# Optimization experiments

Hardware: AMD Instinct MI355X
Metric: run time of the kernel (lower is better)

The kernel has to match this reference:

```python
import jax, jax.numpy as jnp
import numpy as np

B, TQ, TV = 16, 2048, 2048
DEC, ENC = 1024, 512

def setup_inputs() -> dict:
    key = jax.random.key(0)
    k1, k2, k3 = jax.random.split(key, 3)
    query = jax.random.normal(k1, (B, TQ, DEC), dtype=jnp.float32)
    value = jax.random.normal(k2, (B, TV, ENC), dtype=jnp.float32)
    # Dense(decoder_dim): kernel [ENC, DEC] + bias [DEC]
    W = jax.random.normal(k3, (ENC, DEC), dtype=jnp.float32) * (1.0 / np.sqrt(ENC))
    b = jnp.zeros((DEC,), dtype=jnp.float32)
    return {"query": query, "value": value, "W": W, "b": b}

def reference(query, value, W, b):
    # w(value): [B, TV, DEC]
    keys = jnp.einsum('bve,ed->bvd', value, W) + b
    # scores: query @ keys^T -> [B, TQ, TV]
    scores = jnp.einsum('bqd,bvd->bqv', query, keys)
    alignment = jax.nn.softmax(scores, axis=-1)
    # context: alignment @ value -> [B, TQ, ENC]
    context = jnp.einsum('bqv,bve->bqe', alignment, value)
    context = jnp.concatenate([context, query], axis=-1)  # [B, TQ, ENC+DEC]
    alignment_t = jnp.transpose(alignment, (0, 2, 1))      # [B, TV, TQ]
    return (context, alignment_t)
```

## Files before the change

kernel.cpp:

```cpp
#include <hip/hip_runtime.h>
#include <cstdint>
#include <cstddef>

typedef unsigned short u16;
typedef __bf16 bf16x8 __attribute__((ext_vector_type(8)));
typedef unsigned short u16x8 __attribute__((ext_vector_type(8)));
typedef unsigned short u16x4 __attribute__((ext_vector_type(4)));
typedef float f32x4 __attribute__((ext_vector_type(4)));

#define NB   16
#define TQ   2048
#define TV   2048
#define DDEC 1024
#define DENC 512
#define CTXW (DENC + DDEC)
#define CTXW2 (2*CTXW)

static __device__ __forceinline__ u16 f2bf(float f) {
    unsigned u = __builtin_bit_cast(unsigned, f);
    return (u16)((u + 0x7fffu + ((u >> 16) & 1u)) >> 16);
}
static __device__ __forceinline__ float bf2f(u16 h) {
    return __builtin_bit_cast(float, ((unsigned)h) << 16);
}

static __device__ __forceinline__ void stage_tile(
    u16* __restrict__ lds_tile, const u16* __restrict__ gsrc,
    int ldb, int w, int lane)
{
    #pragma unroll
    for (int p = 0; p < 2; ++p) {
        const int ci  = p * 4 + w;
        const int row = ci * 16 + (lane >> 2);
        const int col = (lane & 3) * 8;
        const u16* g = gsrc + (size_t)row * ldb + col;
        u16* l = lds_tile + ci * 512;
        __builtin_amdgcn_global_load_lds(
            (const __attribute__((address_space(1))) void*)g,
            (__attribute__((address_space(3))) void*)l, 16, 0, 0);
    }
}

__global__ __launch_bounds__(256)
void lk_prep_split(const float* __restrict__ X, u16* __restrict__ Xh, u16* __restrict__ Xl)
{
    const size_t i = ((size_t)blockIdx.x * 256 + threadIdx.x) * 4;
    const float4 v = *(const float4*)(X + i);
    const u16 h0=f2bf(v.x), h1=f2bf(v.y), h2=f2bf(v.z), h3=f2bf(v.w);
    u16x4 hv = {h0,h1,h2,h3};
    u16x4 lv = {f2bf(v.x-bf2f(h0)), f2bf(v.y-bf2f(h1)),
                f2bf(v.z-bf2f(h2)), f2bf(v.w-bf2f(h3))};
    *(u16x4*)(Xh + i) = hv;
    *(u16x4*)(Xl + i) = lv;
}

__global__ __launch_bounds__(256)
void lk_prep_vt(const float* __restrict__ V, u16* __restrict__ Vt)
{
    __shared__ float ts[32][36];
    const int t = threadIdx.x;
    const int r = t >> 3, c = (t & 7) * 4;
    const int e0 = blockIdx.x * 32, v0 = blockIdx.y * 32;
    const float* Vb = V + (size_t)blockIdx.z * TV * DENC;
    const float4 v = *(const float4*)(Vb + (size_t)(v0 + r) * DENC + e0 + c);
    *(float4*)&ts[r][c] = v;
    __syncthreads();
    u16x4 tv = { f2bf(ts[c+0][r]), f2bf(ts[c+1][r]),
                 f2bf(ts[c+2][r]), f2bf(ts[c+3][r]) };
    *(u16x4*)(Vt + (size_t)blockIdx.z * DENC * TV + (size_t)(e0 + r) * TV + v0 + c) = tv;
}

__global__ __launch_bounds__(256)
void lk_gemm_qw(const u16* __restrict__ Ah_g, const u16* __restrict__ Al_g,
                const u16* __restrict__ Bh_g, const u16* __restrict__ Bl_g,
                u16* __restrict__ Chi, u16* __restrict__ Clo)
{
    __shared__ u16 lAh[128*32], lAl[128*32], lBh[128*32], lBl[128*32];
    const int m0 = blockIdx.x * 128, n0 = blockIdx.y * 128;
    const int t = threadIdx.x;
    const int w = t >> 6, lane = t & 63, l15 = lane & 15, quad = lane >> 4;

    const u16* Ab_h = Ah_g + (size_t)m0 * DDEC;
    const u16* Ab_l = Al_g + (size_t)m0 * DDEC;
    const u16* Bb_h = Bh_g + (size_t)n0 * DDEC;
    const u16* Bb_l = Bl_g + (size_t)n0 * DDEC;

    f32x4 acc[2][8];
    #pragma unroll
    for (int i = 0; i < 2; ++i)
        #pragma unroll
        for (int j = 0; j < 8; ++j) acc[i][j] = (f32x4){0.f,0.f,0.f,0.f};

    for (int k0 = 0; k0 < DDEC; k0 += 32) {
        stage_tile(lAh, Ab_h + k0, DDEC, w, lane);
        stage_tile(lAl, Ab_l + k0, DDEC, w, lane);
        stage_tile(lBh, Bb_h + k0, DDEC, w, lane);
        stage_tile(lBl, Bb_l + k0, DDEC, w, lane);
        __syncthreads();
        bf16x8 ah[2], al[2];
        #pragma unroll
        for (int tm = 0; tm < 2; ++tm) {
            const int row = w*32 + tm*16 + l15;
            ah[tm] = __builtin_bit_cast(bf16x8, *(const u16x8*)&lAh[row*32 + quad*8]);
            al[tm] = __builtin_bit_cast(bf16x8, *(const u16x8*)&lAl[row*32 + quad*8]);
        }
        #pragma unroll
        for (int tn = 0; tn < 8; ++tn) {
            const int col = tn*16 + l15;
            const bf16x8 bh = __builtin_bit_cast(bf16x8, *(const u16x8*)&lBh[col*32 + quad*8]);
            const bf16x8 bl = __builtin_bit_cast(bf16x8, *(const u16x8*)&lBl[col*32 + quad*8]);
            #pragma unroll
            for (int tm = 0; tm < 2; ++tm) {
                acc[tm][tn] = __builtin_amdgcn_mfma_f32_16x16x32_bf16(ah[tm], bh, acc[tm][tn], 0,0,0);
                acc[tm][tn] = __builtin_amdgcn_mfma_f32_16x16x32_bf16(ah[tm], bl, acc[tm][tn], 0,0,0);
                acc[tm][tn] = __builtin_amdgcn_mfma_f32_16x16x32_bf16(al[tm], bh, acc[tm][tn], 0,0,0);
            }
        }
        __syncthreads();
    }
    #pragma unroll
    for (int tn = 0; tn < 8; ++tn) {
        const int col = n0 + tn*16 + l15;
        #pragma unroll
        for (int tm = 0; tm < 2; ++tm)
            #pragma unroll
            for (int r = 0; r < 4; ++r) {
                const int row = m0 + w*32 + tm*16 + quad*4 + r;
                const float c = acc[tm][tn][r];
                const u16 h = f2bf(c);
                Chi[(size_t)row*DENC + col] = h;
                Clo[(size_t)row*DENC + col] = f2bf(c - bf2f(h));
            }
    }
}

__global__ __launch_bounds__(256)
void lk_gemm_scores(const u16* __restrict__ Ah_g, const u16* __restrict__ Al_g,
                    const u16* __restrict__ Bh_g, const u16* __restrict__ Bl_g,
                    float* __restrict__ Sc, float2* __restrict__ sst)
{
    __shared__ u16 lAh[128*32], lAl[128*32], lBh[128*32], lBl[128*32];
    const int b = blockIdx.z;
    const int m0 = blockIdx.x * 128, n0 = blockIdx.y * 128;
    const int t = threadIdx.x;
    const int w = t >> 6, lane = t & 63, l15 = lane & 15, quad = lane >> 4;

    const u16* Ab_h = Ah_g + (size_t)b * TQ * DENC + (size_t)m0 * DENC;
    const u16* Ab_l = Al_g + (size_t)b * TQ * DENC + (size_t)m0 * DENC;
    const u16* Bb_h = Bh_g + (size_t)b * TV * DENC + (size_t)n0 * DENC;
    const u16* Bb_l = Bl_g + (size_t)b * TV * DENC + (size_t)n0 * DENC;

    f32x4 acc[2][8];
    #pragma unroll
    for (int i = 0; i < 2; ++i)
        #pragma unroll
        for (int j = 0; j < 8; ++j) acc[i][j] = (f32x4){0.f,0.f,0.f,0.f};

    for (int k0 = 0; k0 < DENC; k0 += 32) {
        stage_tile(lAh, Ab_h + k0, DENC, w, lane);
        stage_tile(lAl, Ab_l + k0, DENC, w, lane);
        stage_tile(lBh, Bb_h + k0, DENC, w, lane);
        stage_tile(lBl, Bb_l + k0, DENC, w, lane);
        __syncthreads();
        bf16x8 ah[2], al[2];
        #pragma unroll
        for (int tm = 0; tm < 2; ++tm) {
            const int row = w*32 + tm*16 + l15;
            ah[tm] = __builtin_bit_cast(bf16x8, *(const u16x8*)&lAh[row*32 + quad*8]);
            al[tm] = __builtin_bit_cast(bf16x8, *(const u16x8*)&lAl[row*32 + quad*8]);
        }
        #pragma unroll
        for (int tn = 0; tn < 8; ++tn) {
            const int col = tn*16 + l15;
            const bf16x8 bh = __builtin_bit_cast(bf16x8, *(const u16x8*)&lBh[col*32 + quad*8]);
            const bf16x8 bl = __builtin_bit_cast(bf16x8, *(const u16x8*)&lBl[col*32 + quad*8]);
            #pragma unroll
            for (int tm = 0; tm < 2; ++tm) {
                acc[tm][tn] = __builtin_amdgcn_mfma_f32_16x16x32_bf16(ah[tm], bh, acc[tm][tn], 0,0,0);
                acc[tm][tn] = __builtin_amdgcn_mfma_f32_16x16x32_bf16(ah[tm], bl, acc[tm][tn], 0,0,0);
                acc[tm][tn] = __builtin_amdgcn_mfma_f32_16x16x32_bf16(al[tm], bh, acc[tm][tn], 0,0,0);
            }
        }
        __syncthreads();
    }
    float* Sb = Sc + (size_t)b * TQ * TV;
    #pragma unroll
    for (int tm = 0; tm < 2; ++tm)
        #pragma unroll
        for (int tn = 0; tn < 8; ++tn) {
            const int col = n0 + tn*16 + l15;
            #pragma unroll
            for (int r = 0; r < 4; ++r) {
                const int row = m0 + w*32 + tm*16 + quad*4 + r;
                Sb[(size_t)row*TV + col] = acc[tm][tn][r];
            }
        }
    const int by = blockIdx.y;
    #pragma unroll
    for (int tm = 0; tm < 2; ++tm)
        #pragma unroll
        for (int r = 0; r < 4; ++r) {
            float m = acc[tm][0][r];
            #pragma unroll
            for (int tn = 1; tn < 8; ++tn) m = fmaxf(m, acc[tm][tn][r]);
            #pragma unroll
            for (int off = 1; off < 16; off <<= 1) m = fmaxf(m, __shfl_xor(m, off, 64));
            float s = 0.f;
            #pragma unroll
            for (int tn = 0; tn < 8; ++tn) s += __expf(acc[tm][tn][r] - m);
            #pragma unroll
            for (int off = 1; off < 16; off <<= 1) s += __shfl_xor(s, off, 64);
            if (l15 == 0) {
                const int row = m0 + w*32 + tm*16 + quad*4 + r;
                sst[((size_t)(b*16 + by))*TQ + row] = (float2){m, s};
            }
        }
}

__global__ __launch_bounds__(256)
void lk_combine(float2* __restrict__ sst)
{
    const int rg = blockIdx.x * 256 + threadIdx.x;
    const int b = rg >> 11, q = rg & (TQ - 1);
    float2* base = sst + (size_t)b * 16 * TQ;
    float2 v[16];
    float mx = -3.0e38f;
    #pragma unroll
    for (int y = 0; y < 16; ++y) {
        v[y] = base[(size_t)y * TQ + q];
        mx = fmaxf(mx, v[y].x);
    }
    float s = 0.f;
    #pragma unroll
    for (int y = 0; y < 16; ++y) s += v[y].y * __expf(v[y].x - mx);
    base[q] = (float2){mx, 1.0f / s};
}

__global__ __launch_bounds__(256)
void lk_norm_t(float* __restrict__ A, float* __restrict__ C,
               const float2* __restrict__ sstF)
{
    const int i = blockIdx.x, j = blockIdx.y;
    if (j < i) return;
    const int b = blockIdx.z;
    float* Ab = A + (size_t)b * TQ * TV;
    u16* Pb = (u16*)C + (size_t)b * TQ * CTXW2 + 2*DENC;
    const float2* st = sstF + (size_t)b * 16 * TQ;
    __shared__ float ta[32][36], tb[32][36];
    const int t = threadIdx.x;
    const int r = t >> 3, c = (t & 7) * 4;
    float* pij = Ab + (size_t)(i*32) * TV + j*32;
    float* pji = Ab + (size_t)(j*32) * TV + i*32;
    {
        const float2 s2 = st[i*32 + r];
        const float4 va = *(const float4*)(pij + (size_t)r * TV + c);
        float4 e = { __expf(va.x - s2.x) * s2.y, __expf(va.y - s2.x) * s2.y,
                     __expf(va.z - s2.x) * s2.y, __expf(va.w - s2.x) * s2.y };
        *(float4*)&ta[r][c] = e;
        u16x4 pv = {f2bf(e.x), f2bf(e.y), f2bf(e.z), f2bf(e.w)};
        *(u16x4*)(Pb + (size_t)(i*32 + r) * CTXW2 + j*32 + c) = pv;
    }
    if (i != j) {
        const float2 s2 = st[j*32 + r];
        const float4 vb = *(const float4*)(pji + (size_t)r * TV + c);
        float4 e = { __expf(vb.x - s2.x) * s2.y, __expf(vb.y - s2.x) * s2.y,
                     __expf(vb.z - s2.x) * s2.y, __expf(vb.w - s2.x) * s2.y };
        *(float4*)&tb[r][c] = e;
        u16x4 pv = {f2bf(e.x), f2bf(e.y), f2bf(e.z), f2bf(e.w)};
        *(u16x4*)(Pb + (size_t)(j*32 + r) * CTXW2 + i*32 + c) = pv;
    }
    __syncthreads();
    float4 oa = { ta[c+0][r], ta[c+1][r], ta[c+2][r], ta[c+3][r] };
    *(float4*)(pji + (size_t)r * TV + c) = oa;
    if (i != j) {
        float4 ob = { tb[c+0][r], tb[c+1][r], tb[c+2][r], tb[c+3][r] };
        *(float4*)(pij + (size_t)r * TV + c) = ob;
    }
}

__global__ __launch_bounds__(256)
void lk_gemm_ctx(const u16* __restrict__ Vt, float* C)
{
    __shared__ u16 lA[128*32], lB[128*32];
    const int b = blockIdx.z;
    const int m0 = blockIdx.x * 128, n0 = blockIdx.y * 128;
    const int t = threadIdx.x;
    const int w = t >> 6, lane = t & 63, l15 = lane & 15, quad = lane >> 4;

    const u16* Pb = (const u16*)C + ((size_t)b * TQ + m0) * CTXW2 + 2*DENC;
    const u16* Bb = Vt + (size_t)b * DENC * TV + (size_t)n0 * TV;

    f32x4 acc[2][8];
    #pragma unroll
    for (int i = 0; i < 2; ++i)
        #pragma unroll
        for (int j = 0; j < 8; ++j) acc[i][j] = (f32x4){0.f,0.f,0.f,0.f};

    for (int k0 = 0; k0 < TV; k0 += 32) {
        stage_tile(lA, Pb + k0, CTXW2, w, lane);
        stage_tile(lB, Bb + k0, TV, w, lane);
        __syncthreads();
        bf16x8 af[2];
        #pragma unroll
        for (int tm = 0; tm < 2; ++tm) {
            const int row = w*32 + tm*16 + l15;
            af[tm] = __builtin_bit_cast(bf16x8, *(const u16x8*)&lA[row*32 + quad*8]);
        }
        #pragma unroll
        for (int tn = 0; tn < 8; ++tn) {
            const int col = tn*16 + l15;
            const bf16x8 bf = __builtin_bit_cast(bf16x8, *(const u16x8*)&lB[col*32 + quad*8]);
            #pragma unroll
            for (int tm = 0; tm < 2; ++tm)
                acc[tm][tn] = __builtin_amdgcn_mfma_f32_16x16x32_bf16(af[tm], bf, acc[tm][tn], 0,0,0);
        }
        __syncthreads();
    }
    float* Cb = C + (size_t)b * TQ * CTXW;
    #pragma unroll
    for (int tm = 0; tm < 2; ++tm)
        #pragma unroll
        for (int tn = 0; tn < 8; ++tn) {
            const int col = n0 + tn*16 + l15;
            #pragma unroll
            for (int r = 0; r < 4; ++r) {
                const int row = m0 + w*32 + tm*16 + quad*4 + r;
                Cb[(size_t)row*CTXW + col] = acc[tm][tn][r];
            }
        }
}

__global__ __launch_bounds__(256)
void lk_copy_q(const float* __restrict__ Q, float* __restrict__ C)
{
    const size_t idx = (size_t)blockIdx.x * 256 + threadIdx.x;
    const int d4 = (int)(idx & 255);
    const size_t row = idx >> 8;
    const float4 v = *(const float4*)(Q + (row << 10) + 4*d4);
    *(float4*)(C + row * CTXW + DENC + 4*d4) = v;
}

extern "C" void kernel_launch(void* const* d_in, const int* in_sizes, int n_in,
                              void* d_out, int out_size, void* d_ws, size_t ws_size,
                              hipStream_t stream)
{
    (void)in_sizes; (void)n_in; (void)out_size; (void)ws_size;
    const float* Q = (const float*)d_in[0];
    const float* V = (const float*)d_in[1];
    const float* W = (const float*)d_in[2];
    float* out = (float*)d_out;

    float* ctx   = out;
    float* align = out + (size_t)NB * TQ * CTXW;

    u16* q2h = (u16*)ctx;
    u16* q2l = q2h + (size_t)NB * TQ * DENC;
    u16* vsh = q2l + (size_t)NB * TQ * DENC;
    u16* vsl = vsh + (size_t)NB * TV * DENC;

    u16* qh = (u16*)align;
    u16* ql = qh + (size_t)NB * TQ * DDEC;

    u16* wh = (u16*)d_ws;
    u16* wl = wh + (size_t)DENC * DDEC;
    u16* vt = wl + (size_t)DENC * DDEC;
    float2* sst = (float2*)vt;

    lk_prep_split<<<DENC*DDEC/1024, 256, 0, stream>>>(W, wh, wl);
    lk_prep_split<<<NB*TQ*DDEC/1024, 256, 0, stream>>>(Q, qh, ql);
    lk_prep_split<<<NB*TV*DENC/1024, 256, 0, stream>>>(V, vsh, vsl);
    lk_gemm_qw<<<dim3(NB*TQ/128, DENC/128), 256, 0, stream>>>(qh, ql, wh, wl, q2h, q2l);
    lk_gemm_scores<<<dim3(TQ/128, TV/128, NB), 256, 0, stream>>>(q2h, q2l, vsh, vsl, align, sst);
    lk_combine<<<NB*TQ/256, 256, 0, stream>>>(sst);
    lk_norm_t<<<dim3(TV/32, TV/32, NB), 256, 0, stream>>>(align, ctx, sst);
    lk_prep_vt<<<dim3(DENC/32, TV/32, NB), 256, 0, stream>>>(V, vt);
    lk_gemm_ctx<<<dim3(TQ/128, DENC/128, NB), 256, 0, stream>>>(vt, ctx);
    lk_copy_q<<<NB*TQ*DDEC/1024, 256, 0, stream>>>(Q, ctx);
}
```

Baseline: 1.294 ms.

## Double-buffer LDS tiles in the GEMM kernels to overlap loads with MFMA

The three MFMA GEMM kernels (QW projection, scores and context) now use two LDS buffers each. The next-but-one K tile is issued right after compute, and explicit vmcnt waits plus raw s_barrier calls replace the two __syncthreads per iteration. This is meant to hide global-load latency behind MFMA work instead of stalling on every tile. In exchange, LDS use per block doubles (64 KB in the split-bf16 kernels), which can lower occupancy. Correctness also now depends on the hand-counted vmcnt values matching the number of loads stage_tile issues.

```diff
diff --git a/kernel.cpp b/kernel.cpp
--- a/kernel.cpp
+++ b/kernel.cpp
@@ -15,6 +15,11 @@
 #define DENC 512
 #define CTXW (DENC + DDEC)
 #define CTXW2 (2*CTXW)
+
+#define TILE_U16 4096
+
+#define SBAR()   __builtin_amdgcn_s_barrier()
+#define SCHEDB() __builtin_amdgcn_sched_barrier(0)
 
 static __device__ __forceinline__ u16 f2bf(float f) {
     unsigned u = __builtin_bit_cast(unsigned, f);
@@ -75,7 +80,7 @@
                 const u16* __restrict__ Bh_g, const u16* __restrict__ Bl_g,
                 u16* __restrict__ Chi, u16* __restrict__ Clo)
 {
-    __shared__ u16 lAh[128*32], lAl[128*32], lBh[128*32], lBl[128*32];
+    __shared__ u16 lAh[2*TILE_U16], lAl[2*TILE_U16], lBh[2*TILE_U16], lBl[2*TILE_U16];
     const int m0 = blockIdx.x * 128, n0 = blockIdx.y * 128;
     const int t = threadIdx.x;
     const int w = t >> 6, lane = t & 63, l15 = lane & 15, quad = lane >> 4;
@@ -91,24 +96,37 @@
         #pragma unroll
         for (int j = 0; j < 8; ++j) acc[i][j] = (f32x4){0.f,0.f,0.f,0.f};
 
-    for (int k0 = 0; k0 < DDEC; k0 += 32) {
-        stage_tile(lAh, Ab_h + k0, DDEC, w, lane);
-        stage_tile(lAl, Ab_l + k0, DDEC, w, lane);
-        stage_tile(lBh, Bb_h + k0, DDEC, w, lane);
-        stage_tile(lBl, Bb_l + k0, DDEC, w, lane);
-        __syncthreads();
+    auto stage4 = [&](int buf, int k0) {
+        stage_tile(lAh + buf*TILE_U16, Ab_h + k0, DDEC, w, lane);
+        stage_tile(lAl + buf*TILE_U16, Ab_l + k0, DDEC, w, lane);
+        stage_tile(lBh + buf*TILE_U16, Bb_h + k0, DDEC, w, lane);
+        stage_tile(lBl + buf*TILE_U16, Bb_l + k0, DDEC, w, lane);
+    };
+
+    const int nt = DDEC / 32;
+    stage4(0, 0);
+    stage4(1, 32);
+    for (int it = 0; it < nt; ++it) {
+        const int cur = it & 1;
+        if (it + 1 < nt) { asm volatile("s_waitcnt vmcnt(8)" ::: "memory"); }
+        else             { asm volatile("s_waitcnt vmcnt(0)" ::: "memory"); }
+        SCHEDB(); SBAR(); SCHEDB();
+        const u16* pAh = lAh + cur*TILE_U16;
+        const u16* pAl = lAl + cur*TILE_U16;
+        const u16* pBh = lBh + cur*TILE_U16;
+        const u16* pBl = lBl + cur*TILE_U16;
         bf16x8 ah[2], al[2];
         #pragma unroll
         for (int tm = 0; tm < 2; ++tm) {
             const int row = w*32 + tm*16 + l15;
-            ah[tm] = __builtin_bit_cast(bf16x8, *(const u16x8*)&lAh[row*32 + quad*8]);
-            al[tm] = __builtin_bit_cast(bf16x8, *(const u16x8*)&lAl[row*32 + quad*8]);
+            ah[tm] = __builtin_bit_cast(bf16x8, *(const u16x8*)&pAh[row*32 + quad*8]);
+            al[tm] = __builtin_bit_cast(bf16x8, *(const u16x8*)&pAl[row*32 + quad*8]);
         }
         #pragma unroll
         for (int tn = 0; tn < 8; ++tn) {
             const int col = tn*16 + l15;
-            const bf16x8 bh = __builtin_bit_cast(bf16x8, *(const u16x8*)&lBh[col*32 + quad*8]);
-            const bf16x8 bl = __builtin_bit_cast(bf16x8, *(const u16x8*)&lBl[col*32 + quad*8]);
+            const bf16x8 bh = __builtin_bit_cast(bf16x8, *(const u16x8*)&pBh[col*32 + quad*8]);
+            const bf16x8 bl = __builtin_bit_cast(bf16x8, *(const u16x8*)&pBl[col*32 + quad*8]);
             #pragma unroll
             for (int tm = 0; tm < 2; ++tm) {
                 acc[tm][tn] = __builtin_amdgcn_mfma_f32_16x16x32_bf16(ah[tm], bh, acc[tm][tn], 0,0,0);
@@ -116,7 +134,8 @@
                 acc[tm][tn] = __builtin_amdgcn_mfma_f32_16x16x32_bf16(al[tm], bh, acc[tm][tn], 0,0,0);
             }
         }
-        __syncthreads();
+        SBAR();
+        if (it + 2 < nt) stage4(cur, (it + 2) * 32);
     }
     #pragma unroll
     for (int tn = 0; tn < 8; ++tn) {
@@ -139,7 +158,7 @@
                     const u16* __restrict__ Bh_g, const u16* __restrict__ Bl_g,
                     float* __restrict__ Sc, float2* __restrict__ sst)
 {
-    __shared__ u16 lAh[128*32], lAl[128*32], lBh[128*32], lBl[128*32];
+    __shared__ u16 lAh[2*TILE_U16], lAl[2*TILE_U16], lBh[2*TILE_U16], lBl[2*TILE_U16];
     const int b = blockIdx.z;
     const int m0 = blockIdx.x * 128, n0 = blockIdx.y * 128;
     const int t = threadIdx.x;
@@ -156,24 +175,37 @@
         #pragma unroll
         for (int j = 0; j < 8; ++j) acc[i][j] = (f32x4){0.f,0.f,0.f,0.f};
 
-    for (int k0 = 0; k0 < DENC; k0 += 32) {
-        stage_tile(lAh, Ab_h + k0, DENC, w, lane);
-        stage_tile(lAl, Ab_l + k0, DENC, w, lane);
-        stage_tile(lBh, Bb_h + k0, DENC, w, lane);
-        stage_tile(lBl, Bb_l + k0, DENC, w, lane);
-        __syncthreads();
+    auto stage4 = [&](int buf, int k0) {
+        stage_tile(lAh + buf*TILE_U16, Ab_h + k0, DENC, w, lane);
+        stage_tile(lAl + buf*TILE_U16, Ab_l + k0, DENC, w, lane);
+        stage_tile(lBh + buf*TILE_U16, Bb_h + k0, DENC, w, lane);
+        stage_tile(lBl + buf*TILE_U16, Bb_l + k0, DENC, w, lane);
+    };
+
+    const int nt = DENC / 32;
+    stage4(0, 0);
+    stage4(1, 32);
+    for (int it = 0; it < nt; ++it) {
+        const int cur = it & 1;
+        if (it + 1 < nt) { asm volatile("s_waitcnt vmcnt(8)" ::: "memory"); }
+        else             { asm volatile("s_waitcnt vmcnt(0)" ::: "memory"); }
+        SCHEDB(); SBAR(); SCHEDB();
+        const u16* pAh = lAh + cur*TILE_U16;
+        const u16* pAl = lAl + cur*TILE_U16;
+        const u16* pBh = lBh + cur*TILE_U16;
+        const u16* pBl = lBl + cur*TILE_U16;
         bf16x8 ah[2], al[2];
         #pragma unroll
         for (int tm = 0; tm < 2; ++tm) {
             const int row = w*32 + tm*16 + l15;
-            ah[tm] = __builtin_bit_cast(bf16x8, *(const u16x8*)&lAh[row*32 + quad*8]);
-            al[tm] = __builtin_bit_cast(bf16x8, *(const u16x8*)&lAl[row*32 + quad*8]);
+            ah[tm] = __builtin_bit_cast(bf16x8, *(const u16x8*)&pAh[row*32 + quad*8]);
+            al[tm] = __builtin_bit_cast(bf16x8, *(const u16x8*)&pAl[row*32 + quad*8]);
         }
         #pragma unroll
         for (int tn = 0; tn < 8; ++tn) {
             const int col = tn*16 + l15;
-            const bf16x8 bh = __builtin_bit_cast(bf16x8, *(const u16x8*)&lBh[col*32 + quad*8]);
-            const bf16x8 bl = __builtin_bit_cast(bf16x8, *(const u16x8*)&lBl[col*32 + quad*8]);
+            const bf16x8 bh = __builtin_bit_cast(bf16x8, *(const u16x8*)&pBh[col*32 + quad*8]);
+            const bf16x8 bl = __builtin_bit_cast(bf16x8, *(const u16x8*)&pBl[col*32 + quad*8]);
             #pragma unroll
             for (int tm = 0; tm < 2; ++tm) {
                 acc[tm][tn] = __builtin_amdgcn_mfma_f32_16x16x32_bf16(ah[tm], bh, acc[tm][tn], 0,0,0);
@@ -181,7 +213,8 @@
                 acc[tm][tn] = __builtin_amdgcn_mfma_f32_16x16x32_bf16(al[tm], bh, acc[tm][tn], 0,0,0);
             }
         }
-        __syncthreads();
+        SBAR();
+        if (it + 2 < nt) stage4(cur, (it + 2) * 32);
     }
     float* Sb = Sc + (size_t)b * TQ * TV;
     #pragma unroll
@@ -281,7 +314,7 @@
 __global__ __launch_bounds__(256)
 void lk_gemm_ctx(const u16* __restrict__ Vt, float* C)
 {
-    __shared__ u16 lA[128*32], lB[128*32];
+    __shared__ u16 lA[2*TILE_U16], lB[2*TILE_U16];
     const int b = blockIdx.z;
     const int m0 = blockIdx.x * 128, n0 = blockIdx.y * 128;
     const int t = threadIdx.x;
@@ -296,25 +329,37 @@
         #pragma unroll
         for (int j = 0; j < 8; ++j) acc[i][j] = (f32x4){0.f,0.f,0.f,0.f};
 
-    for (int k0 = 0; k0 < TV; k0 += 32) {
-        stage_tile(lA, Pb + k0, CTXW2, w, lane);
-        stage_tile(lB, Bb + k0, TV, w, lane);
-        __syncthreads();
+    auto stage2 = [&](int buf, int k0) {
+        stage_tile(lA + buf*TILE_U16, Pb + k0, CTXW2, w, lane);
+        stage_tile(lB + buf*TILE_U16, Bb + k0, TV, w, lane);
+    };
+
+    const int nt = TV / 32;
+    stage2(0, 0);
+    stage2(1, 32);
+    for (int it = 0; it < nt; ++it) {
+        const int cur = it & 1;
+        if (it + 1 < nt) { asm volatile("s_waitcnt vmcnt(4)" ::: "memory"); }
+        else             { asm volatile("s_waitcnt vmcnt(0)" ::: "memory"); }
+        SCHEDB(); SBAR(); SCHEDB();
+        const u16* pA = lA + cur*TILE_U16;
+        const u16* pB = lB + cur*TILE_U16;
         bf16x8 af[2];
         #pragma unroll
         for (int tm = 0; tm < 2; ++tm) {
             const int row = w*32 + tm*16 + l15;
-            af[tm] = __builtin_bit_cast(bf16x8, *(const u16x8*)&lA[row*32 + quad*8]);
+            af[tm] = __builtin_bit_cast(bf16x8, *(const u16x8*)&pA[row*32 + quad*8]);
         }
         #pragma unroll
         for (int tn = 0; tn < 8; ++tn) {
             const int col = tn*16 + l15;
-            const bf16x8 bf = __builtin_bit_cast(bf16x8, *(const u16x8*)&lB[col*32 + quad*8]);
+            const bf16x8 bf = __builtin_bit_cast(bf16x8, *(const u16x8*)&pB[col*32 + quad*8]);
             #pragma unroll
             for (int tm = 0; tm < 2; ++tm)
                 acc[tm][tn] = __builtin_amdgcn_mfma_f32_16x16x32_bf16(af[tm], bf, acc[tm][tn], 0,0,0);
         }
-        __syncthreads();
+        SBAR();
+        if (it + 2 < nt) stage2(cur, (it + 2) * 32);
     }
     float* Cb = C + (size_t)b * TQ * CTXW;
     #pragma unroll
```

After: 1.259 ms. -2.7%, faster.
